# Optimization experiments

Hardware: AMD Instinct MI355X
Metric: run time of the kernel (lower is better)

## Reference

```python
import jax, jax.numpy as jnp
import numpy as np
import math

N = 8192
F_IN = 1024
F_OUT = 1024
MAX_ITER = 10


def whale_optimizer(positions, key, max_iter=MAX_ITER):
    """Vectorized whale optimization algorithm.

    Faithful to the original per-agent/per-dim update rules, but the agent
    loop is vectorized (on-device RNG, one parallel update per outer
    iteration); only the `max_iter` outer iterations stay sequential.
    positions: [N, D] float32.
    """
    n, d = positions.shape
    lower = jnp.min(positions)
    upper = jnp.max(positions)
    k0, loop_key = jax.random.split(key)
    leader = positions[jax.random.randint(k0, (), 0, n)]  # [D]

    def step(carry, it):
        pos, leader = carry
        itf = it.astype(jnp.float32)
        k = jax.random.fold_in(loop_key, it)
        k1, k2, k3, k4, k5, k6 = jax.random.split(k, 6)
        a = 2.0 - itf * (2.0 / max_iter)
        a2 = -1.0 + itf * (-1.0 / max_iter)
        r1 = jax.random.uniform(k1, (n, 1))
        r2 = jax.random.uniform(k2, (n, 1))
        A = 2.0 * a * r1 - a                       # [n,1]
        C = 2.0 * r2                               # [n,1]
        lp = (a2 - 1.0) * jax.random.uniform(k3, (n, 1)) + 1.0  # spiral param
        p = jax.random.uniform(k4, (n, 1))
        # random leader per (agent, dim), as in the original inner j-loop
        ridx = jax.random.randint(k5, (n, d), 0, n)
        x_rand = jnp.take_along_axis(pos, ridx, axis=0)         # [n,d]
        explore = jnp.abs(x_rand - A * jnp.abs(C * x_rand - pos))
        exploit = jnp.abs(leader - A * jnp.abs(C * leader - pos))
        spiral = jnp.abs(jnp.abs(leader - pos) * jnp.exp(lp) * jnp.cos(2.0 * jnp.pi * lp) + leader)
        new_pos = jnp.where(p < 0.5,
                            jnp.where(jnp.abs(A) >= 1.0, explore, exploit),
                            spiral)
        new_pos = jnp.clip(new_pos, lower, upper)
        new_leader = new_pos[jax.random.randint(k6, (), 0, n)]
        return (new_pos, new_leader), None

    (positions, _), _ = jax.lax.scan(step, (positions, leader), jnp.arange(max_iter))
    return positions


def setup_inputs() -> dict:
    key = jax.random.key(0)
    k1, k2, k3, k4 = jax.random.split(key, 4)
    stdv = 1.0 / math.sqrt(F_OUT)
    return {
        "input": jax.random.normal(k1, (N, F_IN), dtype=jnp.float32),
        "adj": jax.random.uniform(k2, (N, N), dtype=jnp.float32) * (1.0 / N),
        "h0": jax.random.normal(k3, (N, F_IN), dtype=jnp.float32),
        "weight": jax.random.uniform(k4, (F_IN, F_OUT), dtype=jnp.float32,
                                      minval=-stdv, maxval=stdv),
        "lamda": jnp.float32(0.5),
        "alpha": jnp.float32(0.1),
        "l": 1,
    }


def reference(input, adj, h0, weight, lamda, alpha, l):
    # variant=False, residual=False
    theta = jnp.log(lamda / l + 1.0)
    hi = adj @ input                                  # spmm(adj, input)
    support = (1.0 - alpha) * hi + alpha * h0
    r = support
    # original detaches support before the whale optimizer
    opt = whale_optimizer(jax.lax.stop_gradient(support), jax.random.key(42))
    output = theta * (opt @ weight) + (1.0 - theta) * r
    return output
```

## Files before the change

### kernel.cpp

```cpp
#include <hip/hip_runtime.h>
#include <hip/hip_bf16.h>
#include <stdint.h>
#include <math.h>

typedef uint32_t u32;
typedef __hip_bfloat16 bf16t;
typedef __attribute__((ext_vector_type(8))) short short8;
typedef __attribute__((ext_vector_type(4))) float f32x4;

#define PRNG_MODE 1

__host__ __device__ __forceinline__ void tf2(u32 k0, u32 k1, u32 c0, u32 c1, u32& o0, u32& o1) {
  const u32 ks2 = k0 ^ k1 ^ 0x1BD11BDAu;
  u32 x0 = c0 + k0, x1 = c1 + k1;
#define TFROT(v,r) (((v)<<(r))|((v)>>(32-(r))))
#define TFR(r) { x0 += x1; x1 = TFROT(x1,r); x1 ^= x0; }
  TFR(13) TFR(15) TFR(26) TFR(6)   x0 += k1;  x1 += ks2 + 1u;
  TFR(17) TFR(29) TFR(16) TFR(24)  x0 += ks2; x1 += k0 + 2u;
  TFR(13) TFR(15) TFR(26) TFR(6)   x0 += k0;  x1 += k1 + 3u;
  TFR(17) TFR(29) TFR(16) TFR(24)  x0 += k1;  x1 += ks2 + 4u;
  TFR(13) TFR(15) TFR(26) TFR(6)   x0 += ks2; x1 += k0 + 5u;
#undef TFR
#undef TFROT
  o0 = x0; o1 = x1;
}

__device__ __forceinline__ float unif_row(u32 ka, u32 kb, int i) {
  u32 o0, o1, b;
#if PRNG_MODE == 1
  tf2(ka, kb, 0u, (u32)i, o0, o1); b = o0 ^ o1;
#else
  if (i < 4096) { tf2(ka, kb, (u32)i, (u32)(4096 + i), o0, o1); b = o0; }
  else          { tf2(ka, kb, (u32)(i - 4096), (u32)i, o0, o1); b = o1; }
#endif
  return __uint_as_float(0x3F800000u | (b >> 9)) - 1.0f;
}

__device__ __forceinline__ int ridx_fn(u32 ka, u32 kb, u32 f) {
#if PRNG_MODE == 1
  u32 o0, o1; tf2(ka, kb, 0u, f, o0, o1); return (int)((o0 ^ o1) & 8191u);
#else
  const u32 H = 4194304u;
  u32 o0, o1;
  if (f < H) { tf2(ka, kb, f, H + f, o0, o1); return (int)(o0 & 8191u); }
  tf2(ka, kb, f - H, f, o0, o1); return (int)(o1 & 8191u);
#endif
}

static inline void split2(u32 ka, u32 kb, u32* kA, u32* kB) {
#if PRNG_MODE == 1
  u32 a0, a1, b0, b1;
  tf2(ka, kb, 0u, 0u, a0, a1);
  tf2(ka, kb, 0u, 1u, b0, b1);
  kA[0] = a0; kA[1] = a1; kB[0] = b0; kB[1] = b1;
#else
  u32 a0, a1, b0, b1;
  tf2(ka, kb, 0u, 2u, a0, a1);
  tf2(ka, kb, 1u, 3u, b0, b1);
  kA[0] = a0; kA[1] = b0; kB[0] = a1; kB[1] = b1;
#endif
}

static inline void split6(u32 ka, u32 kb, u32 out[6][2]) {
#if PRNG_MODE == 1
  for (u32 i = 0; i < 6; i++) { u32 o0, o1; tf2(ka, kb, 0u, i, o0, o1); out[i][0] = o0; out[i][1] = o1; }
#else
  u32 xa[6], xb[6];
  for (u32 i = 0; i < 6; i++) tf2(ka, kb, i, 6u + i, xa[i], xb[i]);
  out[0][0] = xa[0]; out[0][1] = xa[1];
  out[1][0] = xa[2]; out[1][1] = xa[3];
  out[2][0] = xa[4]; out[2][1] = xa[5];
  out[3][0] = xb[0]; out[3][1] = xb[1];
  out[4][0] = xb[2]; out[4][1] = xb[3];
  out[5][0] = xb[4]; out[5][1] = xb[5];
#endif
}

static inline int scalar_randint8192(u32 ka, u32 kb) {
  u32 kA[2], kB[2];
  split2(ka, kb, kA, kB);
  u32 o0, o1;
  tf2(kB[0], kB[1], 0u, 0u, o0, o1);
#if PRNG_MODE == 1
  return (int)((o0 ^ o1) & 8191u);
#else
  return (int)(o0 & 8191u);
#endif
}

__device__ __forceinline__ ushort f2bf(float f) {
  u32 u = __float_as_uint(f);
  u32 r = u + 0x7FFFu + ((u >> 16) & 1u);
  return (ushort)(r >> 16);
}

__global__ __launch_bounds__(256) void cvt_k(const float4* __restrict__ x, uint2* __restrict__ y, int n4) {
  for (int i = blockIdx.x * 256 + threadIdx.x; i < n4; i += gridDim.x * 256) {
    float4 v = x[i];
    uint2 o;
    o.x = (u32)f2bf(v.x) | ((u32)f2bf(v.y) << 16);
    o.y = (u32)f2bf(v.z) | ((u32)f2bf(v.w) << 16);
    y[i] = o;
  }
}

__global__ __launch_bounds__(256) void packb_k(const float* __restrict__ B, uint4* __restrict__ out, int K, int Nn) {
  const int idx = blockIdx.x * 256 + threadIdx.x;
  const int total = (K >> 3) * Nn;
  if (idx >= total) return;
  const int g = idx / Nn;
  const int n = idx - g * Nn;
  u32 wv[4];
#pragma unroll
  for (int j = 0; j < 4; j++) {
    const float f0 = B[(size_t)(g * 8 + 2 * j) * Nn + n];
    const float f1 = B[(size_t)(g * 8 + 2 * j + 1) * Nn + n];
    wv[j] = (u32)f2bf(f0) | ((u32)f2bf(f1) << 16);
  }
  uint4 o; o.x = wv[0]; o.y = wv[1]; o.z = wv[2]; o.w = wv[3];
  out[idx] = o;
}

__global__ __launch_bounds__(256) void minmax1_k(const float4* __restrict__ x, int n4, float* __restrict__ part, int G) {
  __shared__ float slo[256], shi[256];
  const int tid = threadIdx.x;
  float lo = 3.4e38f, hi = -3.4e38f;
  for (int i = blockIdx.x * 256 + tid; i < n4; i += G * 256) {
    float4 v = x[i];
    lo = fminf(lo, fminf(fminf(v.x, v.y), fminf(v.z, v.w)));
    hi = fmaxf(hi, fmaxf(fmaxf(v.x, v.y), fmaxf(v.z, v.w)));
  }
  slo[tid] = lo; shi[tid] = hi; __syncthreads();
  for (int s = 128; s > 0; s >>= 1) {
    if (tid < s) { slo[tid] = fminf(slo[tid], slo[tid + s]); shi[tid] = fmaxf(shi[tid], shi[tid + s]); }
    __syncthreads();
  }
  if (tid == 0) { part[blockIdx.x] = slo[0]; part[G + blockIdx.x] = shi[0]; }
}

__global__ __launch_bounds__(256) void minmax2_k(const float* __restrict__ part, int G, float* __restrict__ bnd) {
  __shared__ float slo[256], shi[256];
  const int tid = threadIdx.x;
  float lo = 3.4e38f, hi = -3.4e38f;
  for (int i = tid; i < G; i += 256) { lo = fminf(lo, part[i]); hi = fmaxf(hi, part[G + i]); }
  slo[tid] = lo; shi[tid] = hi; __syncthreads();
  for (int s = 128; s > 0; s >>= 1) {
    if (tid < s) { slo[tid] = fminf(slo[tid], slo[tid + s]); shi[tid] = fmaxf(shi[tid], shi[tid + s]); }
    __syncthreads();
  }
  if (tid == 0) { bnd[0] = slo[0]; bnd[1] = shi[0]; }
}

__device__ __forceinline__ void gld_lds16(const void* g, void* l) {
  __builtin_amdgcn_global_load_lds((const __attribute__((address_space(1))) void*)g,
                                   (__attribute__((address_space(3))) void*)l, 16, 0, 0);
}

template <int EPI>
__global__ __launch_bounds__(256) void gemm_k(
    const bf16t* __restrict__ A, const bf16t* __restrict__ Bp,
    const float* __restrict__ aux, const float* __restrict__ sF,
    const int* __restrict__ sI, float* __restrict__ C, int Nn, int K) {
  __shared__ __align__(16) bf16t As[128 * 32];
  __shared__ __align__(16) bf16t Bs[128 * 32];
  const int tid = threadIdx.x;
  const int lane = tid & 63;
  const int wave = tid >> 6;
  const int nb = Nn >> 7;
  const int bm = blockIdx.x / nb;
  const int bn = blockIdx.x - bm * nb;
  const int m0 = bm << 7, n0 = bn << 7;
  const int wm = (wave & 1) << 6, wn = (wave >> 1) << 6;

  f32x4 acc[4][4];
#pragma unroll
  for (int i = 0; i < 4; i++)
#pragma unroll
    for (int j = 0; j < 4; j++) acc[i][j] = (f32x4){0.f, 0.f, 0.f, 0.f};

  const int uA0 = tid, uA1 = tid + 256;
  const bf16t* gA0 = A + (size_t)(m0 + (uA0 >> 2)) * K + ((uA0 & 3) << 3);
  const bf16t* gA1 = A + (size_t)(m0 + (uA1 >> 2)) * K + ((uA1 & 3) << 3);
  bf16t* lA0 = As + (uA0 << 3);
  bf16t* lA1 = As + (uA1 << 3);
  const bf16t* gB0 = Bp + ((size_t)(uA0 >> 7) * Nn + n0 + (uA0 & 127)) * 8;
  const bf16t* gB1 = Bp + ((size_t)(uA1 >> 7) * Nn + n0 + (uA1 & 127)) * 8;
  bf16t* lB0 = Bs + (uA0 << 3);
  bf16t* lB1 = Bs + (uA1 << 3);
  const size_t bstep = (size_t)Nn * 32;

  for (int k0 = 0; k0 < K; k0 += 32) {
    __syncthreads();
    gld_lds16(gA0 + k0, lA0);
    gld_lds16(gA1 + k0, lA1);
    gld_lds16(gB0, lB0);
    gld_lds16(gB1, lB1);
    gB0 += bstep; gB1 += bstep;
    __syncthreads();
    const int arow = lane & 15, aq = lane >> 4;
    short8 af[4], bfv[4];
#pragma unroll
    for (int mt = 0; mt < 4; mt++)
      af[mt] = *(const short8*)(As + ((wm + mt * 16 + arow) << 5) + (aq << 3));
#pragma unroll
    for (int nt = 0; nt < 4; nt++)
      bfv[nt] = *(const short8*)(Bs + (((aq << 7) + wn + nt * 16 + arow) << 3));
#pragma unroll
    for (int mt = 0; mt < 4; mt++)
#pragma unroll
      for (int nt = 0; nt < 4; nt++)
        acc[mt][nt] = __builtin_amdgcn_mfma_f32_16x16x32_bf16(af[mt], bfv[nt], acc[mt][nt], 0, 0, 0);
  }

  float p1, p2;
  if (EPI == 1) { const float al = sF[0]; p1 = 1.0f - al; p2 = al; }
  else { const float th = logf(sF[0] / (float)sI[0] + 1.0f); p1 = th; p2 = 1.0f - th; }
  const int col = lane & 15, rq = lane >> 4;
#pragma unroll
  for (int mt = 0; mt < 4; mt++)
#pragma unroll
    for (int nt = 0; nt < 4; nt++)
#pragma unroll
      for (int r = 0; r < 4; r++) {
        const int gm = m0 + wm + mt * 16 + (rq << 2) + r;
        const int gn = n0 + wn + nt * 16 + col;
        const size_t ix = (size_t)gm * Nn + gn;
        C[ix] = p1 * acc[mt][nt][r] + p2 * aux[ix];
      }
}

struct WA {
  u32 k1a, k1b, k2a, k2b, k3a, k3b, k4a, k4b, k5a, k5b;
  int ldr;
  float a, a2;
};

__global__ __launch_bounds__(256) void whale_k(
    const float* __restrict__ pinb, float* __restrict__ poutb,
    ushort* __restrict__ opt, const float* __restrict__ bnd, WA w) {
  const int row = blockIdx.x;
  const int tid = threadIdx.x;
  __shared__ float sh[4];
  if (tid < 4) {
    u32 ka, kb;
    if (tid == 0)      { ka = w.k1a; kb = w.k1b; }
    else if (tid == 1) { ka = w.k2a; kb = w.k2b; }
    else if (tid == 2) { ka = w.k3a; kb = w.k3b; }
    else               { ka = w.k4a; kb = w.k4b; }
    sh[tid] = unif_row(ka, kb, row);
  }
  __syncthreads();
  const float r1 = sh[0], r2 = sh[1], u3 = sh[2], p = sh[3];
  float t2 = (2.0f * w.a) * r1;
  asm volatile("" : "+v"(t2));
  const float A = t2 - w.a;
  const float Cc = 2.0f * r2;
  const float lo = bnd[0], hi = bnd[1];
  const float* pin = pinb + ((size_t)row << 10);
  const int j0 = tid << 2;
  float4 pv = *(const float4*)(pin + j0);
  float ov[4];
  const bool bp = (p < 0.5f);
  if (bp && (fabsf(A) >= 1.0f)) {
    const u32 fb = ((u32)row << 10) + (u32)j0;
#pragma unroll
    for (int e = 0; e < 4; e++) {
      const float pos = (&pv.x)[e];
      const int ri = ridx_fn(w.k5a, w.k5b, fb + (u32)e);
      const float xr = pinb[((size_t)ri << 10) + j0 + e];
      ov[e] = fabsf(xr - A * fabsf(Cc * xr - pos));
    }
  } else {
    const float* ldp = pinb + ((size_t)w.ldr << 10);
    float4 lv = *(const float4*)(ldp + j0);
    if (bp) {
#pragma unroll
      for (int e = 0; e < 4; e++) {
        const float pos = (&pv.x)[e], ld = (&lv.x)[e];
        ov[e] = fabsf(ld - A * fabsf(Cc * ld - pos));
      }
    } else {
      const float lp = (w.a2 - 1.0f) * u3 + 1.0f;
      const float s1 = expf(lp);
      const float s2 = cosf(6.2831855f * lp);
#pragma unroll
      for (int e = 0; e < 4; e++) {
        const float pos = (&pv.x)[e], ld = (&lv.x)[e];
        ov[e] = fabsf(fabsf(ld - pos) * s1 * s2 + ld);
      }
    }
  }
  float4 res;
#pragma unroll
  for (int e = 0; e < 4; e++) (&res.x)[e] = fminf(fmaxf(ov[e], lo), hi);
  *(float4*)(poutb + ((size_t)row << 10) + j0) = res;
  if (opt) {
    ushort4 o4;
    o4.x = f2bf(res.x); o4.y = f2bf(res.y); o4.z = f2bf(res.z); o4.w = f2bf(res.w);
    *(ushort4*)(opt + ((size_t)row << 10) + j0) = o4;
  }
}

extern "C" void kernel_launch(void* const* d_in, const int* in_sizes, int n_in,
                              void* d_out, int out_size, void* d_ws, size_t ws_size,
                              hipStream_t stream) {
  const float* inp = (const float*)d_in[0];
  const float* adj = (const float*)d_in[1];
  const float* h0  = (const float*)d_in[2];
  const float* wgt = (const float*)d_in[3];
  const float* lam = (const float*)d_in[4];
  const float* alp = (const float*)d_in[5];
  const int* lint  = (const int*)d_in[6];
  float* outp = (float*)d_out;

  char* ws = (char*)d_ws;
  bf16t* Abf  = (bf16t*)(ws);
  float* P0   = (float*)(ws);
  float* P1   = (float*)(ws + 33554432);
  ushort* OPT = (ushort*)(ws + 67108864);
  bf16t* B1p  = (bf16t*)(ws + 134217728);
  bf16t* Wp   = (bf16t*)(ws + 150994944);
  float* SUP  = (float*)(ws + 153092096);
  float* PRT  = (float*)(ws + 186646528);
  float* BND  = (float*)(ws + 186662912);

  hipLaunchKernelGGL(cvt_k, dim3(4096), dim3(256), 0, stream, (const float4*)adj, (uint2*)Abf, 16777216);
  hipLaunchKernelGGL(packb_k, dim3(4096), dim3(256), 0, stream, inp, (uint4*)B1p, 8192, 1024);
  hipLaunchKernelGGL(packb_k, dim3(512), dim3(256), 0, stream, wgt, (uint4*)Wp, 1024, 1024);
  hipLaunchKernelGGL((gemm_k<1>), dim3(512), dim3(256), 0, stream, Abf, B1p, h0, alp, lint, SUP, 1024, 8192);
  hipLaunchKernelGGL(minmax1_k, dim3(2048), dim3(256), 0, stream, (const float4*)SUP, 2097152, PRT, 2048);
  hipLaunchKernelGGL(minmax2_k, dim3(1), dim3(256), 0, stream, PRT, 2048, BND);

  u32 k0k[2], lpk[2];
  split2(0u, 42u, k0k, lpk);
  int ldr = scalar_randint8192(k0k[0], k0k[1]);
  const float* cur = SUP;
  float* bufs[2] = {P0, P1};
  for (int it = 0; it < 10; ++it) {
    u32 ka, kb; tf2(lpk[0], lpk[1], 0u, (u32)it, ka, kb);
    u32 ks[6][2];
    split6(ka, kb, ks);
    u32 k5A[2], k5B[2];
    split2(ks[4][0], ks[4][1], k5A, k5B);
    WA w;
    w.k1a = ks[0][0]; w.k1b = ks[0][1];
    w.k2a = ks[1][0]; w.k2b = ks[1][1];
    w.k3a = ks[2][0]; w.k3b = ks[2][1];
    w.k4a = ks[3][0]; w.k4b = ks[3][1];
    w.k5a = k5B[0];   w.k5b = k5B[1];
    w.ldr = ldr;
    const float itf = (float)it;
    w.a = 2.0f - itf * 0.2f;
    w.a2 = -1.0f + itf * (-0.1f);
    float* nxt = bufs[it & 1];
    hipLaunchKernelGGL(whale_k, dim3(8192), dim3(256), 0, stream, cur, nxt,
                       (it == 9) ? OPT : (ushort*)nullptr, BND, w);
    cur = nxt;
    ldr = scalar_randint8192(ks[5][0], ks[5][1]);
  }
  hipLaunchKernelGGL((gemm_k<2>), dim3(512), dim3(256), 0, stream, (const bf16t*)OPT, Wp, SUP, lam, lint, outp, 1024, 1024);
  (void)in_sizes; (void)n_in; (void)out_size; (void)ws_size;
}
```

Measured before the change: 956.6 us.

## Fuse min/max reduction into first GEMM epilogue and use 512-thread blocks

Removes the separate minmax1 pass over the 32MB support matrix by computing per-block min/max in the GEMM epilogue and writing partials for a single final reduction. The GEMM block grows to 512 threads (8 waves), each wave covering a 64x32 sub-tile, so every thread issues one A load and one B load per k-step instead of two each. The block-to-tile mapping becomes column-major over M. It also strips the unused alternate PRNG mode. Costs are an extra LDS tree reduction with barriers in the epilogue and fewer accumulators per wave, which lowers MFMA reuse per fragment load.

Measured after the change: 907.5 us. 1.05x faster.

```diff
diff --git a/kernel.cpp b/kernel.cpp
--- a/kernel.cpp
+++ b/kernel.cpp
@@ -8,7 +8,6 @@
 typedef __attribute__((ext_vector_type(8))) short short8;
 typedef __attribute__((ext_vector_type(4))) float f32x4;
 
-#define PRNG_MODE 1
 
 __host__ __device__ __forceinline__ void tf2(u32 k0, u32 k1, u32 c0, u32 c1, u32& o0, u32& o1) {
   const u32 ks2 = k0 ^ k1 ^ 0x1BD11BDAu;
@@ -26,54 +25,24 @@
 }
 
 __device__ __forceinline__ float unif_row(u32 ka, u32 kb, int i) {
-  u32 o0, o1, b;
-#if PRNG_MODE == 1
-  tf2(ka, kb, 0u, (u32)i, o0, o1); b = o0 ^ o1;
-#else
-  if (i < 4096) { tf2(ka, kb, (u32)i, (u32)(4096 + i), o0, o1); b = o0; }
-  else          { tf2(ka, kb, (u32)(i - 4096), (u32)i, o0, o1); b = o1; }
-#endif
-  return __uint_as_float(0x3F800000u | (b >> 9)) - 1.0f;
+  u32 o0, o1;
+  tf2(ka, kb, 0u, (u32)i, o0, o1);
+  return __uint_as_float(0x3F800000u | ((o0 ^ o1) >> 9)) - 1.0f;
 }
 
 __device__ __forceinline__ int ridx_fn(u32 ka, u32 kb, u32 f) {
-#if PRNG_MODE == 1
   u32 o0, o1; tf2(ka, kb, 0u, f, o0, o1); return (int)((o0 ^ o1) & 8191u);
-#else
-  const u32 H = 4194304u;
-  u32 o0, o1;
-  if (f < H) { tf2(ka, kb, f, H + f, o0, o1); return (int)(o0 & 8191u); }
-  tf2(ka, kb, f - H, f, o0, o1); return (int)(o1 & 8191u);
-#endif
 }
 
 static inline void split2(u32 ka, u32 kb, u32* kA, u32* kB) {
-#if PRNG_MODE == 1
   u32 a0, a1, b0, b1;
   tf2(ka, kb, 0u, 0u, a0, a1);
   tf2(ka, kb, 0u, 1u, b0, b1);
   kA[0] = a0; kA[1] = a1; kB[0] = b0; kB[1] = b1;
-#else
-  u32 a0, a1, b0, b1;
-  tf2(ka, kb, 0u, 2u, a0, a1);
-  tf2(ka, kb, 1u, 3u, b0, b1);
-  kA[0] = a0; kA[1] = b0; kB[0] = a1; kB[1] = b1;
-#endif
 }
 
 static inline void split6(u32 ka, u32 kb, u32 out[6][2]) {
-#if PRNG_MODE == 1
   for (u32 i = 0; i < 6; i++) { u32 o0, o1; tf2(ka, kb, 0u, i, o0, o1); out[i][0] = o0; out[i][1] = o1; }
-#else
-  u32 xa[6], xb[6];
-  for (u32 i = 0; i < 6; i++) tf2(ka, kb, i, 6u + i, xa[i], xb[i]);
-  out[0][0] = xa[0]; out[0][1] = xa[1];
-  out[1][0] = xa[2]; out[1][1] = xa[3];
-  out[2][0] = xa[4]; out[2][1] = xa[5];
-  out[3][0] = xb[0]; out[3][1] = xb[1];
-  out[4][0] = xb[2]; out[4][1] = xb[3];
-  out[5][0] = xb[4]; out[5][1] = xb[5];
-#endif
 }
 
 static inline int scalar_randint8192(u32 ka, u32 kb) {
@@ -81,11 +50,7 @@
   split2(ka, kb, kA, kB);
   u32 o0, o1;
   tf2(kB[0], kB[1], 0u, 0u, o0, o1);
-#if PRNG_MODE == 1
   return (int)((o0 ^ o1) & 8191u);
-#else
-  return (int)(o0 & 8191u);
-#endif
 }
 
 __device__ __forceinline__ ushort f2bf(float f) {
@@ -119,23 +84,6 @@
   }
   uint4 o; o.x = wv[0]; o.y = wv[1]; o.z = wv[2]; o.w = wv[3];
   out[idx] = o;
-}
-
-__global__ __launch_bounds__(256) void minmax1_k(const float4* __restrict__ x, int n4, float* __restrict__ part, int G) {
-  __shared__ float slo[256], shi[256];
-  const int tid = threadIdx.x;
-  float lo = 3.4e38f, hi = -3.4e38f;
-  for (int i = blockIdx.x * 256 + tid; i < n4; i += G * 256) {
-    float4 v = x[i];
-    lo = fminf(lo, fminf(fminf(v.x, v.y), fminf(v.z, v.w)));
-    hi = fmaxf(hi, fmaxf(fmaxf(v.x, v.y), fmaxf(v.z, v.w)));
-  }
-  slo[tid] = lo; shi[tid] = hi; __syncthreads();
-  for (int s = 128; s > 0; s >>= 1) {
-    if (tid < s) { slo[tid] = fminf(slo[tid], slo[tid + s]); shi[tid] = fmaxf(shi[tid], shi[tid + s]); }
-    __syncthreads();
-  }
-  if (tid == 0) { part[blockIdx.x] = slo[0]; part[G + blockIdx.x] = shi[0]; }
 }
 
 __global__ __launch_bounds__(256) void minmax2_k(const float* __restrict__ part, int G, float* __restrict__ bnd) {
@@ -157,58 +105,52 @@
 }
 
 template <int EPI>
-__global__ __launch_bounds__(256) void gemm_k(
+__global__ __launch_bounds__(512, 4) void gemm_k(
     const bf16t* __restrict__ A, const bf16t* __restrict__ Bp,
     const float* __restrict__ aux, const float* __restrict__ sF,
-    const int* __restrict__ sI, float* __restrict__ C, int Nn, int K) {
+    const int* __restrict__ sI, float* __restrict__ C,
+    float* __restrict__ prt, int PG, int Nn, int K) {
   __shared__ __align__(16) bf16t As[128 * 32];
   __shared__ __align__(16) bf16t Bs[128 * 32];
   const int tid = threadIdx.x;
   const int lane = tid & 63;
   const int wave = tid >> 6;
-  const int nb = Nn >> 7;
-  const int bm = blockIdx.x / nb;
-  const int bn = blockIdx.x - bm * nb;
+  const int bm = blockIdx.x & 63;
+  const int bn = blockIdx.x >> 6;
   const int m0 = bm << 7, n0 = bn << 7;
-  const int wm = (wave & 1) << 6, wn = (wave >> 1) << 6;
-
-  f32x4 acc[4][4];
+  const int wm = (wave & 1) << 6;
+  const int wn = (wave >> 1) << 5;
+
+  f32x4 acc[4][2];
 #pragma unroll
   for (int i = 0; i < 4; i++)
 #pragma unroll
-    for (int j = 0; j < 4; j++) acc[i][j] = (f32x4){0.f, 0.f, 0.f, 0.f};
-
-  const int uA0 = tid, uA1 = tid + 256;
-  const bf16t* gA0 = A + (size_t)(m0 + (uA0 >> 2)) * K + ((uA0 & 3) << 3);
-  const bf16t* gA1 = A + (size_t)(m0 + (uA1 >> 2)) * K + ((uA1 & 3) << 3);
-  bf16t* lA0 = As + (uA0 << 3);
-  bf16t* lA1 = As + (uA1 << 3);
-  const bf16t* gB0 = Bp + ((size_t)(uA0 >> 7) * Nn + n0 + (uA0 & 127)) * 8;
-  const bf16t* gB1 = Bp + ((size_t)(uA1 >> 7) * Nn + n0 + (uA1 & 127)) * 8;
-  bf16t* lB0 = Bs + (uA0 << 3);
-  bf16t* lB1 = Bs + (uA1 << 3);
+    for (int j = 0; j < 2; j++) acc[i][j] = (f32x4){0.f, 0.f, 0.f, 0.f};
+
+  const bf16t* gA = A + (size_t)(m0 + (tid >> 2)) * K + ((tid & 3) << 3);
+  bf16t* lA = As + (tid << 3);
+  const bf16t* gB = Bp + ((size_t)(tid >> 7) * Nn + n0 + (tid & 127)) * 8;
+  bf16t* lB = Bs + (tid << 3);
   const size_t bstep = (size_t)Nn * 32;
 
   for (int k0 = 0; k0 < K; k0 += 32) {
     __syncthreads();
-    gld_lds16(gA0 + k0, lA0);
-    gld_lds16(gA1 + k0, lA1);
-    gld_lds16(gB0, lB0);
-    gld_lds16(gB1, lB1);
-    gB0 += bstep; gB1 += bstep;
+    gld_lds16(gA + k0, lA);
+    gld_lds16(gB, lB);
+    gB += bstep;
     __syncthreads();
     const int arow = lane & 15, aq = lane >> 4;
-    short8 af[4], bfv[4];
+    short8 af[4], bfv[2];
 #pragma unroll
     for (int mt = 0; mt < 4; mt++)
       af[mt] = *(const short8*)(As + ((wm + mt * 16 + arow) << 5) + (aq << 3));
 #pragma unroll
-    for (int nt = 0; nt < 4; nt++)
+    for (int nt = 0; nt < 2; nt++)
       bfv[nt] = *(const short8*)(Bs + (((aq << 7) + wn + nt * 16 + arow) << 3));
 #pragma unroll
     for (int mt = 0; mt < 4; mt++)
 #pragma unroll
-      for (int nt = 0; nt < 4; nt++)
+      for (int nt = 0; nt < 2; nt++)
         acc[mt][nt] = __builtin_amdgcn_mfma_f32_16x16x32_bf16(af[mt], bfv[nt], acc[mt][nt], 0, 0, 0);
   }
 
@@ -216,17 +158,34 @@
   if (EPI == 1) { const float al = sF[0]; p1 = 1.0f - al; p2 = al; }
   else { const float th = logf(sF[0] / (float)sI[0] + 1.0f); p1 = th; p2 = 1.0f - th; }
   const int col = lane & 15, rq = lane >> 4;
+  float vlo = 3.4e38f, vhi = -3.4e38f;
 #pragma unroll
   for (int mt = 0; mt < 4; mt++)
 #pragma unroll
-    for (int nt = 0; nt < 4; nt++)
+    for (int nt = 0; nt < 2; nt++)
 #pragma unroll
       for (int r = 0; r < 4; r++) {
         const int gm = m0 + wm + mt * 16 + (rq << 2) + r;
         const int gn = n0 + wn + nt * 16 + col;
         const size_t ix = (size_t)gm * Nn + gn;
-        C[ix] = p1 * acc[mt][nt][r] + p2 * aux[ix];
+        const float v = p1 * acc[mt][nt][r] + p2 * aux[ix];
+        C[ix] = v;
+        if (EPI == 1) { vlo = fminf(vlo, v); vhi = fmaxf(vhi, v); }
       }
+  if (EPI == 1) {
+    __syncthreads();
+    float* red = (float*)As;
+    red[tid] = vlo; red[512 + tid] = vhi;
+    __syncthreads();
+    for (int s = 256; s > 0; s >>= 1) {
+      if (tid < s) {
+        red[tid] = fminf(red[tid], red[tid + s]);
+        red[512 + tid] = fmaxf(red[512 + tid], red[512 + tid + s]);
+      }
+      __syncthreads();
+    }
+    if (tid == 0) { prt[blockIdx.x] = red[0]; prt[PG + blockIdx.x] = red[512]; }
+  }
 }
 
 struct WA {
@@ -327,9 +286,8 @@
   hipLaunchKernelGGL(cvt_k, dim3(4096), dim3(256), 0, stream, (const float4*)adj, (uint2*)Abf, 16777216);
   hipLaunchKernelGGL(packb_k, dim3(4096), dim3(256), 0, stream, inp, (uint4*)B1p, 8192, 1024);
   hipLaunchKernelGGL(packb_k, dim3(512), dim3(256), 0, stream, wgt, (uint4*)Wp, 1024, 1024);
-  hipLaunchKernelGGL((gemm_k<1>), dim3(512), dim3(256), 0, stream, Abf, B1p, h0, alp, lint, SUP, 1024, 8192);
-  hipLaunchKernelGGL(minmax1_k, dim3(2048), dim3(256), 0, stream, (const float4*)SUP, 2097152, PRT, 2048);
-  hipLaunchKernelGGL(minmax2_k, dim3(1), dim3(256), 0, stream, PRT, 2048, BND);
+  hipLaunchKernelGGL((gemm_k<1>), dim3(512), dim3(512), 0, stream, Abf, B1p, h0, alp, lint, SUP, PRT, 512, 1024, 8192);
+  hipLaunchKernelGGL(minmax2_k, dim3(1), dim3(256), 0, stream, PRT, 512, BND);
 
   u32 k0k[2], lpk[2];
   split2(0u, 42u, k0k, lpk);
@@ -358,6 +316,7 @@
     cur = nxt;
     ldr = scalar_randint8192(ks[5][0], ks[5][1]);
   }
-  hipLaunchKernelGGL((gemm_k<2>), dim3(512), dim3(256), 0, stream, (const bf16t*)OPT, Wp, SUP, lam, lint, outp, 1024, 1024);
+  hipLaunchKernelGGL((gemm_k<2>), dim3(512), dim3(512), 0, stream, (const bf16t*)OPT, Wp, SUP, lam, lint, outp,
+                     (float*)nullptr, 0, 1024, 1024);
   (void)in_sizes; (void)n_in; (void)out_size; (void)ws_size;
 }
```
